# Kernel tuning notes

Hardware: AMD Instinct MI355X
Metric: run time of the kernel (lower is better)

## Reference

```python
import jax, jax.numpy as jnp
import numpy as np

KH, KW = 3, 3          # kernel_size
SH, SW = 1, 1          # stride
PH, PW = 1, 1          # padding
NCODEBOOKS = 16
SUBVEC = 36            # (64*3*3)/16
K = 16                 # codewords per codebook (4 tree levels)


def _unfold(x):
    """torch.nn.functional.unfold equivalent: (b,c,h,w) -> (b, c*KH*KW, oh, ow),
    feature dim ordered channel-major (c, ki, kj) like torch."""
    b, c, h, w = x.shape
    xp = jnp.pad(x, ((0, 0), (0, 0), (PH, PH), (PW, PW)))
    oh = (h + 2 * PH - KH) // SH + 1
    ow = (w + 2 * PW - KW) // SW + 1
    patches = [xp[:, :, i:i + (oh - 1) * SH + 1:SH, j:j + (ow - 1) * SW + 1:SW]
               for i in range(KH) for j in range(KW)]
    cols = jnp.stack(patches, axis=2)              # (b, c, KH*KW, oh, ow)
    return cols.reshape(b, c * KH * KW, oh, ow)


def setup_inputs() -> dict:
    key = jax.random.key(0)
    k1, k2, k3, k4, k5 = jax.random.split(key, 5)
    return {
        "x": jax.random.normal(k1, (16, 64, 56, 56), dtype=jnp.float32),
        "split_idxs": jax.random.randint(k2, (NCODEBOOKS, 4), 0, SUBVEC, dtype=jnp.int32),
        "split_vals": jax.random.normal(k3, (NCODEBOOKS, 4, K // 2), dtype=jnp.float32),
        "lookup_tables": jax.random.normal(k4, (NCODEBOOKS, K, 64), dtype=jnp.float32),
        "bias": jax.random.normal(k5, (64,), dtype=jnp.float32),
    }


def reference(x, split_idxs, split_vals, lookup_tables, bias):
    b = x.shape[0]
    cols = _unfold(x)                              # (b, d, oh, ow)
    _, d, oh, ow = cols.shape
    # torch: cols.permute(0,2,1).flatten(0,1) with L=oh*ow row-major
    xf = cols.reshape(b, d, oh * ow).transpose(0, 2, 1).reshape(-1, d)  # (n, d)
    n = xf.shape[0]
    xs = xf.reshape(n, NCODEBOOKS, SUBVEC)
    car = jnp.arange(NCODEBOOKS)
    # Hierarchical 4-level threshold encoding (vectorized over all codebooks):
    # at level t, a point in bucket e compares feature split_idxs[c,t] against
    # split_vals[c,t,e]; new bucket = 2*e + (v >= thr)  (matches the serial
    # bucket-list construction: '<' -> left child, '>=' -> right child).
    enc = jnp.zeros((n, NCODEBOOKS), dtype=jnp.int32)
    for t in range(4):
        v = xs[:, car, split_idxs[:, t]]           # (n, NCODEBOOKS)
        thr = split_vals[car[None, :], t, enc]     # (n, NCODEBOOKS)
        enc = 2 * enc + (v >= thr).astype(jnp.int32)
    # LUT gather-sum (equivalent to one_hot(enc) @ lookup_tables[i], summed)
    gathered = lookup_tables[car[None, :], enc]    # (n, NCODEBOOKS, out_ch)
    out = gathered.sum(axis=1) + bias              # (n, out_ch)
    out = out.reshape(b, oh, ow, -1).transpose(0, 3, 1, 2)
    return out
```

## Files before the change

kernel.cpp:

```cpp
#include <hip/hip_runtime.h>
#include <hip/hip_fp16.h>

static constexpr int W56 = 56;
static constexpr int SP  = 56 * 56;
static constexpr int CHN = 64;

__device__ __forceinline__ float rfl_f(float v) {
    return __int_as_float(__builtin_amdgcn_readfirstlane(__float_as_int(v)));
}

__global__ __launch_bounds__(256, 3) void maddness_conv(
    const float* __restrict__ x,
    const int*   __restrict__ si,
    const float* __restrict__ sv,
    const float* __restrict__ lut,
    const float* __restrict__ bias,
    float*       __restrict__ out)
{
    __shared__ __half2        lutLds[256 * 36];
    __shared__ unsigned short codes[256];

    const int tid  = threadIdx.x;
    const int part = tid >> 6;
    const int lane = tid & 63;

    const int b  = blockIdx.x / 49;
    const int s  = (blockIdx.x - b * 49) * 64 + lane;
    const int y  = s / W56;
    const int xc = s - y * W56;
    const float* __restrict__ xb = x + b * (CHN * SP);

    float v[4][4];
    #pragma unroll
    for (int c = 0; c < 4; ++c) {
        #pragma unroll
        for (int t = 0; t < 4; ++t) {
            const int cb = part * 4 + c;
            const int i  = cb * 4 + t;
            const int g  = __builtin_amdgcn_readfirstlane(si[i]) + cb * 36;
            const int ch = g / 9;
            const int k9 = g - ch * 9;
            const int ki = k9 / 3;
            const int dy = ki - 1;
            const int dx = (k9 - ki * 3) - 1;
            const int yy = y + dy, xx = xc + dx;
            const bool ok = ((unsigned)yy < (unsigned)W56) & ((unsigned)xx < (unsigned)W56);
            const int yyc = min(max(yy, 0), W56 - 1);
            const int xxc = min(max(xx, 0), W56 - 1);
            const float lv = xb[ch * SP + yyc * W56 + xxc];
            v[c][t] = ok ? lv : 0.0f;
        }
    }

    float T0[4], T1[4][2], T2[4][4], T3[4][8];
    #pragma unroll
    for (int c = 0; c < 4; ++c) {
        const int base = (part * 4 + c) * 32;
        T0[c] = rfl_f(sv[base]);
        #pragma unroll
        for (int j = 0; j < 2; ++j) T1[c][j] = rfl_f(sv[base + 8  + j]);
        #pragma unroll
        for (int j = 0; j < 4; ++j) T2[c][j] = rfl_f(sv[base + 16 + j]);
        #pragma unroll
        for (int j = 0; j < 8; ++j) T3[c][j] = rfl_f(sv[base + 24 + j]);
    }

    const float4* lut4 = reinterpret_cast<const float4*>(lut);
    #pragma unroll
    for (int i = 0; i < 16; ++i) {
        const int idx = tid + i * 256;
        const int row = idx >> 4, k = idx & 15;
        const float4 f = lut4[idx];
        lutLds[row * 36 + 2 * k]     = __float22half2_rn(make_float2(f.x, f.y));
        lutLds[row * 36 + 2 * k + 1] = __float22half2_rn(make_float2(f.z, f.w));
    }

    unsigned code = 0;
    #pragma unroll
    for (int c = 0; c < 4; ++c) {
        const bool b0 = v[c][0] >= T0[c];
        const float t1 = b0 ? T1[c][1] : T1[c][0];
        const bool b1 = v[c][1] >= t1;
        const float s01 = b1 ? T2[c][1] : T2[c][0];
        const float s23 = b1 ? T2[c][3] : T2[c][2];
        const bool b2 = v[c][2] >= (b0 ? s23 : s01);
        const float w0 = b2 ? T3[c][1] : T3[c][0];
        const float w1 = b2 ? T3[c][3] : T3[c][2];
        const float w2 = b2 ? T3[c][5] : T3[c][4];
        const float w3 = b2 ? T3[c][7] : T3[c][6];
        const float z0 = b1 ? w1 : w0;
        const float z1 = b1 ? w3 : w2;
        const bool b3 = v[c][3] >= (b0 ? z1 : z0);
        const int e = ((int)b0 << 3) | ((int)b1 << 2) | ((int)b2 << 1) | (int)b3;
        code |= (unsigned)e << (4 * c);
    }
    codes[part * 64 + lane] = (unsigned short)code;
    __syncthreads();

    const int q = part;
    const unsigned cd0 = codes[lane];
    const unsigned cd1 = codes[64 + lane];
    const unsigned cd2 = codes[128 + lane];
    const unsigned cd3 = codes[192 + lane];

    __half2 acc[8];
    #pragma unroll
    for (int r = 0; r < 8; ++r) acc[r] = __half2{__half(0.0f), __half(0.0f)};

    #pragma unroll
    for (int cb = 0; cb < 16; ++cb) {
        const unsigned cw = (cb < 4) ? cd0 : (cb < 8) ? cd1 : (cb < 12) ? cd2 : cd3;
        const int e = (int)((cw >> ((cb & 3) * 4)) & 15u);
        const __half2* __restrict__ row = &lutLds[(cb * 16 + e) * 36 + q * 8];
        #pragma unroll
        for (int r = 0; r < 8; ++r) acc[r] += row[r];
    }

    float* __restrict__ op = out + b * (CHN * SP) + (q * 16) * SP + s;
    const float* __restrict__ bq = bias + q * 16;
    #pragma unroll
    for (int r = 0; r < 8; ++r) {
        const float2 f = __half22float2(acc[r]);
        op[(2 * r)     * SP] = f.x + bq[2 * r];
        op[(2 * r + 1) * SP] = f.y + bq[2 * r + 1];
    }
}

extern "C" void kernel_launch(void* const* d_in, const int* in_sizes, int n_in,
                              void* d_out, int out_size, void* d_ws, size_t ws_size,
                              hipStream_t stream) {
    const float* x  = (const float*)d_in[0];
    const int*   si = (const int*)  d_in[1];
    const float* sv = (const float*)d_in[2];
    const float* lt = (const float*)d_in[3];
    const float* bs = (const float*)d_in[4];
    float* o = (float*)d_out;

    maddness_conv<<<dim3(784), dim3(256), 0, stream>>>(x, si, sv, lt, bs, o);
}
```

Measured before the change: 77.47 us.

## Split fused kernel into separate encode and LUT-decode kernels via workspace

```diff
diff --git a/kernel.cpp b/kernel.cpp
--- a/kernel.cpp
+++ b/kernel.cpp
@@ -4,28 +4,36 @@
 static constexpr int W56 = 56;
 static constexpr int SP  = 56 * 56;
 static constexpr int CHN = 64;
+static constexpr int NPT = 16 * SP;
 
 __device__ __forceinline__ float rfl_f(float v) {
     return __int_as_float(__builtin_amdgcn_readfirstlane(__float_as_int(v)));
 }
 
-__global__ __launch_bounds__(256, 3) void maddness_conv(
+__global__ __launch_bounds__(256) void k_encode(
     const float* __restrict__ x,
     const int*   __restrict__ si,
     const float* __restrict__ sv,
     const float* __restrict__ lut,
-    const float* __restrict__ bias,
-    float*       __restrict__ out)
+    __half2*        __restrict__ lutH2,
+    unsigned short* __restrict__ codes)
 {
-    __shared__ __half2        lutLds[256 * 36];
-    __shared__ unsigned short codes[256];
-
     const int tid  = threadIdx.x;
     const int part = tid >> 6;
     const int lane = tid & 63;
 
-    const int b  = blockIdx.x / 49;
-    const int s  = (blockIdx.x - b * 49) * 64 + lane;
+    if (blockIdx.x == 0) {
+        const float2* l2 = reinterpret_cast<const float2*>(lut);
+        #pragma unroll
+        for (int k = 0; k < 32; ++k) {
+            const int idx = tid + k * 256;
+            lutH2[idx] = __float22half2_rn(l2[idx]);
+        }
+    }
+
+    const int p  = blockIdx.x * 64 + lane;
+    const int b  = p / SP;
+    const int s  = p - b * SP;
     const int y  = s / W56;
     const int xc = s - y * W56;
     const float* __restrict__ xb = x + b * (CHN * SP);
@@ -65,16 +73,6 @@
         for (int j = 0; j < 8; ++j) T3[c][j] = rfl_f(sv[base + 24 + j]);
     }
 
-    const float4* lut4 = reinterpret_cast<const float4*>(lut);
-    #pragma unroll
-    for (int i = 0; i < 16; ++i) {
-        const int idx = tid + i * 256;
-        const int row = idx >> 4, k = idx & 15;
-        const float4 f = lut4[idx];
-        lutLds[row * 36 + 2 * k]     = __float22half2_rn(make_float2(f.x, f.y));
-        lutLds[row * 36 + 2 * k + 1] = __float22half2_rn(make_float2(f.z, f.w));
-    }
-
     unsigned code = 0;
     #pragma unroll
     for (int c = 0; c < 4; ++c) {
@@ -94,14 +92,39 @@
         const int e = ((int)b0 << 3) | ((int)b1 << 2) | ((int)b2 << 1) | (int)b3;
         code |= (unsigned)e << (4 * c);
     }
-    codes[part * 64 + lane] = (unsigned short)code;
+    codes[part * NPT + p] = (unsigned short)code;
+}
+
+__global__ __launch_bounds__(256, 3) void k_decode(
+    const __half2*        __restrict__ lutH2,
+    const unsigned short* __restrict__ codes,
+    const float*          __restrict__ bias,
+    float*                __restrict__ out)
+{
+    __shared__ __half2 lutLds[256 * 36];
+
+    const int tid  = threadIdx.x;
+    const int q    = tid >> 6;
+    const int lane = tid & 63;
+
+    const int p = blockIdx.x * 64 + lane;
+    const int b = p / SP;
+    const int s = p - b * SP;
+
+    const unsigned cd0 = codes[p];
+    const unsigned cd1 = codes[NPT + p];
+    const unsigned cd2 = codes[2 * NPT + p];
+    const unsigned cd3 = codes[3 * NPT + p];
+
+    const float4* src = reinterpret_cast<const float4*>(lutH2);
+    #pragma unroll
+    for (int i = 0; i < 8; ++i) {
+        const int idx   = tid + i * 256;
+        const int row   = idx >> 3;
+        const int chunk = idx & 7;
+        *reinterpret_cast<float4*>(&lutLds[row * 36 + chunk * 4]) = src[idx];
+    }
     __syncthreads();
-
-    const int q = part;
-    const unsigned cd0 = codes[lane];
-    const unsigned cd1 = codes[64 + lane];
-    const unsigned cd2 = codes[128 + lane];
-    const unsigned cd3 = codes[192 + lane];
 
     __half2 acc[8];
     #pragma unroll
@@ -136,5 +159,9 @@
     const float* bs = (const float*)d_in[4];
     float* o = (float*)d_out;
 
-    maddness_conv<<<dim3(784), dim3(256), 0, stream>>>(x, si, sv, lt, bs, o);
+    __half2*        lutH2 = (__half2*)d_ws;
+    unsigned short* codes = (unsigned short*)((char*)d_ws + 32768);
+
+    k_encode<<<dim3(784), dim3(256), 0, stream>>>(x, si, sv, lt, lutH2, codes);
+    k_decode<<<dim3(784), dim3(256), 0, stream>>>(lutH2, codes, bs, o);
 }
```

Result: slower. 79.40 us (+2.5%).
